# Optimization experiments

Measured on AMD Instinct MI355X. Metric: run time of the kernel, lower is better.

## Reference

```python
import jax, jax.numpy as jnp
import numpy as np

THETA = 10000.0

def _rope(x, cos, sin):
    # x: [B, S, D]; cos/sin: [S, D/2]. Pairs are (x[..., 2i], x[..., 2i+1]) treated as complex.
    xr = x.reshape(*x.shape[:-1], -1, 2)
    x0, x1 = xr[..., 0], xr[..., 1]
    o0 = x0 * cos - x1 * sin
    o1 = x0 * sin + x1 * cos
    return jnp.stack([o0, o1], axis=-1).reshape(x.shape)

def setup_inputs() -> dict:
    key = jax.random.key(0)
    ks = jax.random.split(key, 7)
    B, S, D = 4, 2048, 1024
    sd = 1.0 / np.sqrt(D)
    return {
        "x": jax.random.normal(ks[0], (B, S, D), dtype=jnp.float32),
        "wq_w": jax.random.normal(ks[1], (D, D), dtype=jnp.float32) * sd,
        "wq_b": jax.random.normal(ks[2], (D,), dtype=jnp.float32) * 0.01,
        "wk_w": jax.random.normal(ks[3], (D, D), dtype=jnp.float32) * sd,
        "wk_b": jax.random.normal(ks[4], (D,), dtype=jnp.float32) * 0.01,
        "wv_w": jax.random.normal(ks[5], (D, D), dtype=jnp.float32) * sd,
        "wv_b": jax.random.normal(ks[6], (D,), dtype=jnp.float32) * 0.01,
    }

def reference(x, wq_w, wq_b, wk_w, wk_b, wv_w, wv_b):
    B, S, D = x.shape
    # QKV projections (torch Linear: y = x @ W.T + b)
    q = jnp.einsum('bsd,ed->bse', x, wq_w) + wq_b
    k = jnp.einsum('bsd,ed->bse', x, wk_w) + wk_b
    v = jnp.einsum('bsd,ed->bse', x, wv_w) + wv_b
    # Rotary embedding: freqs_cis[t, i] = exp(i * t / theta^(2i/D))
    inv_freq = 1.0 / (THETA ** (jnp.arange(0, D, 2, dtype=jnp.float32) / D))  # [D/2]
    ang = jnp.arange(S, dtype=jnp.float32)[:, None] * inv_freq[None, :]  # [S, D/2]
    cos, sin = jnp.cos(ang), jnp.sin(ang)
    q = _rope(q, cos, sin)
    k = _rope(k, cos, sin)
    # Full (non-causal, single-head) attention with scale 1/sqrt(dim)
    scores = jnp.einsum('bqd,bkd->bqk', q, k) / jnp.sqrt(jnp.float32(D))
    probs = jax.nn.softmax(scores.astype(jnp.float32), axis=-1)
    return jnp.einsum('bqk,bkd->bqd', probs, v)
```

## Files before the change

### kernel.cpp

```cpp
#include <hip/hip_runtime.h>
#include <cstdint>

using u16 = unsigned short;
using u32 = unsigned int;

typedef __attribute__((ext_vector_type(8))) short short8;
typedef __attribute__((ext_vector_type(4))) float floatx4;

__device__ __forceinline__ u16 f2bf(float f) {
    u32 u = __float_as_uint(f);
    u32 r = u + 0x7fffu + ((u >> 16) & 1u);
    return (u16)(r >> 16);
}

__global__ void cvt_all(const float* __restrict__ x, u16* __restrict__ xb,
                        const float* __restrict__ w0, const float* __restrict__ w1,
                        const float* __restrict__ w2,
                        u16* __restrict__ o0, u16* __restrict__ o1, u16* __restrict__ o2,
                        const float* __restrict__ qb, const float* __restrict__ kb,
                        float* __restrict__ bqk, float* __restrict__ rowsum)
{
    int b = blockIdx.x;
    if (b >= 11272) {
        long i = ((long)(b - 11272) * 256 + threadIdx.x) * 4;
        *reinterpret_cast<float4*>(rowsum + i) = make_float4(0.f, 0.f, 0.f, 0.f);
        return;
    }
    if (b >= 11264) {
        int i = (b - 11264) * 256 + threadIdx.x;
        bqk[i] = (i < 1024) ? qb[i] : kb[i - 1024];
        return;
    }
    const float* src; u16* dst; long base;
    if (b < 8192) { src = x; dst = xb; base = (long)b; }
    else {
        int r = b - 8192, seg = r >> 10;
        if (seg == 0)      { src = w0; dst = o0; }
        else if (seg == 1) { src = w1; dst = o1; }
        else               { src = w2; dst = o2; }
        base = (long)(r & 1023);
    }
    long i = (base * 256 + threadIdx.x) * 4;
    float4 v = *reinterpret_cast<const float4*>(src + i);
    uint2 o;
    o.x = (u32)f2bf(v.x) | ((u32)f2bf(v.y) << 16);
    o.y = (u32)f2bf(v.z) | ((u32)f2bf(v.w) << 16);
    *reinterpret_cast<uint2*>(dst + i) = o;
}

__device__ __forceinline__ void async_cp16(const u16* g, u16* l) {
    __builtin_amdgcn_global_load_lds(
        (const __attribute__((address_space(1))) void*)g,
        (__attribute__((address_space(3))) void*)l, 16, 0, 0);
}

#define MEMFENCE asm volatile("" ::: "memory")
__device__ __forceinline__ void barrier_raw() {
    MEMFENCE; __builtin_amdgcn_s_barrier(); MEMFENCE;
}
__device__ __forceinline__ void vmwait(int n) {
    if      (n == 6) asm volatile("s_waitcnt vmcnt(6)" ::: "memory");
    else if (n == 4) asm volatile("s_waitcnt vmcnt(4)" ::: "memory");
    else if (n == 2) asm volatile("s_waitcnt vmcnt(2)" ::: "memory");
    else if (n == 0) asm volatile("s_waitcnt vmcnt(0)" ::: "memory");
}

template <bool BF16_OUT, bool EXPOUT>
__device__ __forceinline__ void gemm_core(
    const u16* __restrict__ A, const u16* __restrict__ B, void* __restrict__ Cv,
    int K, int lda, int ldb, int ldc,
    long tile_m, long tile_n, long cbase,
    const float* bias_col, const float* bias_row,
    float scale, bool rope, float* __restrict__ rowsum,
    const float* __restrict__ rowscale, u16* smem)
{
    u16* As = smem;
    u16* Bs = smem + 8192;

    const int tid  = threadIdx.x;
    const int lane = tid & 63;
    const int wave = tid >> 6;
    const int wm = (wave >> 1) << 6;
    const int wn = (wave & 1) << 6;

    floatx4 acc[4][4] = {};

    const int srow = tid >> 2;
    const int skp  = (((tid & 3) ^ (srow & 3))) * 8;
    const u16* Ag = A + (tile_m + srow) * (long)lda + skp;
    const u16* Bg = B + (tile_n + srow) * (long)ldb + skp;
    u16* Asl = &As[tid * 8];
    u16* Bsl = &Bs[tid * 8];

    const int fm  = lane & 15;
    const int fks = (((lane >> 4) ^ (lane & 3))) * 8;

    for (int k0 = 0; k0 < K; k0 += 64) {
        async_cp16(Ag,                       Asl);
        async_cp16(Ag + 64 * (long)lda,      Asl + 64 * 32);
        async_cp16(Ag + 32,                  Asl + 4096);
        async_cp16(Ag + 32 + 64 * (long)lda, Asl + 4096 + 64 * 32);
        async_cp16(Bg,                       Bsl);
        async_cp16(Bg + 64 * (long)ldb,      Bsl + 64 * 32);
        async_cp16(Bg + 32,                  Bsl + 4096);
        async_cp16(Bg + 32 + 64 * (long)ldb, Bsl + 4096 + 64 * 32);
        Ag += 64; Bg += 64;
        __syncthreads();

        #pragma unroll
        for (int c = 0; c < 2; ++c) {
            const u16* Ap = As + c * 4096;
            const u16* Bp = Bs + c * 4096;
            short8 af[4], bfr[4];
            #pragma unroll
            for (int i = 0; i < 4; ++i)
                af[i] = *reinterpret_cast<const short8*>(&Ap[(wm + i * 16 + fm) * 32 + fks]);
            #pragma unroll
            for (int j = 0; j < 4; ++j)
                bfr[j] = *reinterpret_cast<const short8*>(&Bp[(wn + j * 16 + fm) * 32 + fks]);
            #pragma unroll
            for (int i = 0; i < 4; ++i)
                #pragma unroll
                for (int j = 0; j < 4; ++j)
                    acc[i][j] = __builtin_amdgcn_mfma_f32_16x16x32_bf16(af[i], bfr[j], acc[i][j], 0, 0, 0);
        }
        __syncthreads();
    }

    const int q4  = lane >> 4;
    const int c16 = lane & 15;
    float* smemf  = (float*)smem;
    float* myeps = smemf + wave * (16 * 68);
    const long n0 = tile_n + wn + c16 * 4;

    float4 bc4 = make_float4(0.f, 0.f, 0.f, 0.f);
    if (bias_col) bc4 = *reinterpret_cast<const float4*>(bias_col + n0);

    float inv0 = 0.f, inv1 = 0.f;
    if (rope) {
        int p0 = (int)(n0 >> 1);
        inv0 = __expf((float)(p0 & 511)       * -1.79889463e-2f);
        inv1 = __expf((float)((p0 + 1) & 511) * -1.79889463e-2f);
    }

    #pragma unroll
    for (int i = 0; i < 4; ++i) {
        #pragma unroll
        for (int j = 0; j < 4; ++j)
            #pragma unroll
            for (int r = 0; r < 4; ++r)
                myeps[(q4 * 4 + r) * 68 + j * 16 + c16] = acc[i][j][r];
        __syncthreads();
        #pragma unroll
        for (int p = 0; p < 4; ++p) {
            int lrow = p * 4 + q4;
            long m = tile_m + wm + i * 16 + lrow;
            float4 v = *reinterpret_cast<const float4*>(&myeps[lrow * 68 + c16 * 4]);
            float sc = scale;
            if (rowscale) sc *= 1.0f / rowscale[m];
            v.x = v.x * sc + bc4.x;
            v.y = v.y * sc + bc4.y;
            v.z = v.z * sc + bc4.z;
            v.w = v.w * sc + bc4.w;
            if (bias_row) {
                float br = bias_row[m];
                v.x += br; v.y += br; v.z += br; v.w += br;
            }
            if (rope) {
                int s = (int)(m & 2047);
                float a0 = (float)s * inv0, a1 = (float)s * inv1;
                float sn0 = __sinf(a0), cs0 = __cosf(a0);
                float sn1 = __sinf(a1), cs1 = __cosf(a1);
                float x0 = v.x, x1 = v.y, x2 = v.z, x3 = v.w;
                v.x = x0 * cs0 - x1 * sn0;
                v.y = x0 * sn0 + x1 * cs0;
                v.z = x2 * cs1 - x3 * sn1;
                v.w = x2 * sn1 + x3 * cs1;
            }
            if constexpr (EXPOUT) {
                v.x = __expf(v.x); v.y = __expf(v.y);
                v.z = __expf(v.z); v.w = __expf(v.w);
                float s4 = v.x + v.y + v.z + v.w;
                s4 += __shfl_xor(s4, 1);
                s4 += __shfl_xor(s4, 2);
                s4 += __shfl_xor(s4, 4);
                s4 += __shfl_xor(s4, 8);
                if (c16 == 0) atomicAdd(&rowsum[m], s4);
            }
            long off = cbase + m * (long)ldc + n0;
            if constexpr (BF16_OUT) {
                uint2 o;
                o.x = (u32)f2bf(v.x) | ((u32)f2bf(v.y) << 16);
                o.y = (u32)f2bf(v.z) | ((u32)f2bf(v.w) << 16);
                *reinterpret_cast<uint2*>((u16*)Cv + off) = o;
            } else {
                *reinterpret_cast<float4*>((float*)Cv + off) = v;
            }
        }
        __syncthreads();
    }
}

template <bool BF16_OUT, bool EXPOUT>
__device__ __forceinline__ void gemm8_core(
    const u16* __restrict__ A, const u16* __restrict__ B, void* __restrict__ Cv,
    int K, int lda, int ldb, int ldc,
    long tile_m, long tile_n, long cbase,
    const float* __restrict__ bias_col, const float* __restrict__ bias_row,
    float scale, bool rope, float* __restrict__ rowsum, u16* smem)
{
    const int tid  = threadIdx.x;
    const int lane = tid & 63;
    const int wave = tid >> 6;
    const int wm2  = (wave >> 2) * 128;
    const int wn2  = (wave & 3) * 64;
    const int fm   = lane & 15;
    const int fks  = (((lane >> 4) ^ ((lane >> 1) & 3))) * 8;

    const int srow = tid >> 2;
    const int kgl  = ((tid & 3) ^ ((tid >> 3) & 3)) * 8;
    const u16* Asrc = A + (tile_m + srow) * (long)lda + kgl;
    const u16* Bsrc = B + (tile_n + srow) * (long)ldb + kgl;
    u16* dst0 = smem + tid * 8;

    const int U = K >> 5;

    floatx4 acc[8][4] = {};
    short8 bf[4];

    auto stageA = [&](int v) {
        u16* d = dst0 + ((2 * v) & 7) * 8192;
        const u16* s = Asrc + v * 32;
        async_cp16(s, d);
        async_cp16(s + 128 * (long)lda, d + 4096);
    };
    auto stageB = [&](int v) {
        u16* d = dst0 + ((2 * v + 1) & 7) * 8192;
        const u16* s = Bsrc + v * 32;
        async_cp16(s, d);
        async_cp16(s + 128 * (long)ldb, d + 4096);
    };

    auto phase_pair = [&](int u, int vmx, bool stb, bool sta)
        __attribute__((always_inline))
    {
        const u16* Ap = smem + ((2 * u) & 7) * 8192;
        const u16* Bp = smem + ((2 * u + 1) & 7) * 8192;
        short8 af[4];
        #pragma unroll
        for (int i = 0; i < 4; ++i)
            af[i] = *reinterpret_cast<const short8*>(&Ap[(wm2 + i * 16 + fm) * 32 + fks]);
        #pragma unroll
        for (int j = 0; j < 4; ++j)
            bf[j] = *reinterpret_cast<const short8*>(&Bp[(wn2 + j * 16 + fm) * 32 + fks]);
        if (stb) stageB(u + 2);
        vmwait(vmx);
        barrier_raw();
        __builtin_amdgcn_sched_barrier(0);
        __builtin_amdgcn_s_setprio(1);
        #pragma unroll
        for (int i = 0; i < 4; ++i)
            #pragma unroll
            for (int j = 0; j < 4; ++j)
                acc[i][j] = __builtin_amdgcn_mfma_f32_16x16x32_bf16(af[i], bf[j], acc[i][j], 0, 0, 0);
        __builtin_amdgcn_s_setprio(0);
        __builtin_amdgcn_sched_barrier(0);
        barrier_raw();
        #pragma unroll
        for (int i = 0; i < 4; ++i)
            af[i] = *reinterpret_cast<const short8*>(&Ap[(wm2 + 64 + i * 16 + fm) * 32 + fks]);
        if (sta) stageA(u + 3);
        barrier_raw();
        __builtin_amdgcn_sched_barrier(0);
        __builtin_amdgcn_s_setprio(1);
        #pragma unroll
        for (int i = 0; i < 4; ++i)
            #pragma unroll
            for (int j = 0; j < 4; ++j)
                acc[4 + i][j] = __builtin_amdgcn_mfma_f32_16x16x32_bf16(af[i], bf[j], acc[4 + i][j], 0, 0, 0);
        __builtin_amdgcn_s_setprio(0);
        __builtin_amdgcn_sched_barrier(0);
        barrier_raw();
    };

    stageA(0); stageB(0); stageA(1); stageB(1); stageA(2);
    vmwait(6);
    barrier_raw();

    for (int u = 0; u + 3 < U; ++u)
        phase_pair(u, 6, true, true);
    phase_pair(U - 3, 6, true,  false);
    phase_pair(U - 2, 2, false, false);
    phase_pair(U - 1, 0, false, false);

    const int q4  = lane >> 4;
    const int c16 = lane & 15;
    float* smemf  = (float*)smem;
    float* myeps  = smemf + wave * (16 * 68);
    const long n0 = tile_n + wn2 + c16 * 4;

    float4 bc4 = make_float4(0.f, 0.f, 0.f, 0.f);
    if (bias_col) bc4 = *reinterpret_cast<const float4*>(bias_col + n0);

    float inv0 = 0.f, inv1 = 0.f;
    if (rope) {
        int p0 = (int)(n0 >> 1);
        inv0 = __expf((float)(p0 & 511)       * -1.79889463e-2f);
        inv1 = __expf((float)((p0 + 1) & 511) * -1.79889463e-2f);
    }

    #pragma unroll
    for (int i = 0; i < 8; ++i) {
        #pragma unroll
        for (int j = 0; j < 4; ++j)
            #pragma unroll
            for (int r = 0; r < 4; ++r)
                myeps[(q4 * 4 + r) * 68 + j * 16 + c16] = acc[i][j][r];
        __syncthreads();
        #pragma unroll
        for (int p = 0; p < 4; ++p) {
            int lrow = p * 4 + q4;
            long m = tile_m + wm2 + i * 16 + lrow;
            float4 v = *reinterpret_cast<const float4*>(&myeps[lrow * 68 + c16 * 4]);
            v.x = v.x * scale + bc4.x;
            v.y = v.y * scale + bc4.y;
            v.z = v.z * scale + bc4.z;
            v.w = v.w * scale + bc4.w;
            if (bias_row) {
                float br = bias_row[m];
                v.x += br; v.y += br; v.z += br; v.w += br;
            }
            if (rope) {
                int s = (int)(m & 2047);
                float a0 = (float)s * inv0, a1 = (float)s * inv1;
                float sn0 = __sinf(a0), cs0 = __cosf(a0);
                float sn1 = __sinf(a1), cs1 = __cosf(a1);
                float x0 = v.x, x1 = v.y, x2 = v.z, x3 = v.w;
                v.x = x0 * cs0 - x1 * sn0;
                v.y = x0 * sn0 + x1 * cs0;
                v.z = x2 * cs1 - x3 * sn1;
                v.w = x2 * sn1 + x3 * cs1;
            }
            if constexpr (EXPOUT) {
                v.x = __expf(v.x); v.y = __expf(v.y);
                v.z = __expf(v.z); v.w = __expf(v.w);
                float s4 = v.x + v.y + v.z + v.w;
                s4 += __shfl_xor(s4, 1);
                s4 += __shfl_xor(s4, 2);
                s4 += __shfl_xor(s4, 4);
                s4 += __shfl_xor(s4, 8);
                if (c16 == 0) atomicAdd(&rowsum[m], s4);
            }
            long off = cbase + m * (long)ldc + n0;
            if constexpr (BF16_OUT) {
                uint2 o;
                o.x = (u32)f2bf(v.x) | ((u32)f2bf(v.y) << 16);
                o.y = (u32)f2bf(v.z) | ((u32)f2bf(v.w) << 16);
                *reinterpret_cast<uint2*>((u16*)Cv + off) = o;
            } else {
                *reinterpret_cast<float4*>((float*)Cv + off) = v;
            }
        }
        __syncthreads();
    }
}

__global__ __launch_bounds__(256, 4)
void gemm_fused12(const u16* __restrict__ xb, const u16* __restrict__ wqk,
                  const u16* __restrict__ wv, u16* __restrict__ QK, u16* __restrict__ VT,
                  const float* __restrict__ bqk, const float* __restrict__ wvb)
{
    u32 id = blockIdx.x;
    id = (id & 7u) * 192u + (id >> 3);
    __shared__ alignas(16) u16 smem[16384];
    if (id < 1024u) {
        u32 bx = id & 15u, by = id >> 4;
        gemm_core<true, false>(xb, wqk, QK, 1024, 1024, 1024, 2048,
                        (long)by * 128, (long)bx * 128, 0L,
                        bqk, nullptr, 1.0f, true, nullptr, nullptr, smem);
    } else {
        u32 r = id - 1024u;
        u32 bx = r & 15u, by = (r >> 4) & 7u, bz = r >> 7;
        gemm_core<true, false>(wv, xb + (long)bz * 2048 * 1024, VT,
                        1024, 1024, 1024, 2048,
                        (long)by * 128, (long)bx * 128, (long)bz * 1024 * 2048,
                        nullptr, wvb, 1.0f, false, nullptr, nullptr, smem);
    }
}

__global__ __launch_bounds__(512, 2)
void gemm8_qkt(const u16* __restrict__ QK, u16* __restrict__ Pbuf,
               float* __restrict__ rsum)
{
    u32 id = blockIdx.x;
    id = (id & 7u) * 32u + (id >> 3);
    u32 bz = id >> 6, q = id & 63u, bx = q & 7u, by = q >> 3;
    __shared__ alignas(16) u16 smem[65536];
    const u16* base = QK + (long)bz * 2048 * 2048;
    gemm8_core<true, true>(base, base + 1024, Pbuf, 1024, 2048, 2048, 2048,
                           nullptr == nullptr ? (long)by * 256 : 0, (long)bx * 256,
                           (long)bz * 2048 * 2048,
                           nullptr, nullptr, 0.03125f, false,
                           rsum + (long)bz * 2048, smem);
}

__global__ __launch_bounds__(256, 4)
void gemm_pv(const u16* __restrict__ Pbuf, const u16* __restrict__ VT,
             float* __restrict__ out, const float* __restrict__ rsum)
{
    u32 ord = blockIdx.x;
    u32 x  = ord & 7u;
    u32 n  = ord >> 3;
    u32 bz = x >> 1;
    u32 by = (x & 1u) * 8u + (n >> 3);
    u32 bx = n & 7u;
    __shared__ alignas(16) u16 smem[16384];
    gemm_core<false, false>(Pbuf + (long)bz * 2048 * 2048,
                            VT   + (long)bz * 1024 * 2048,
                            out, 2048, 2048, 2048, 1024,
                            (long)by * 128, (long)bx * 128, (long)bz * 2048 * 1024,
                            nullptr, nullptr, 1.0f, false, nullptr,
                            rsum + (long)bz * 2048, smem);
}

extern "C" void kernel_launch(void* const* d_in, const int* in_sizes, int n_in,
                              void* d_out, int out_size, void* d_ws, size_t ws_size,
                              hipStream_t stream)
{
    const float* x   = (const float*)d_in[0];
    const float* wqw = (const float*)d_in[1];
    const float* wqb = (const float*)d_in[2];
    const float* wkw = (const float*)d_in[3];
    const float* wkb = (const float*)d_in[4];
    const float* wvw = (const float*)d_in[5];
    const float* wvb = (const float*)d_in[6];
    float* out = (float*)d_out;

    char* ws = (char*)d_ws;
    const size_t MB = 1ull << 20;
    u16*   Pbuf = (u16*)(ws + 64 * MB);
    u16*   QK   = (u16*)(ws + 96 * MB);
    u16*   VT   = (u16*)(ws + 128 * MB);
    float* rsum = (float*)(ws + 144 * MB);
    u16*   xb    = (u16*)(ws + 0);
    u16*   wqk   = (u16*)(ws + 16 * MB);
    u16*   wvbuf = (u16*)(ws + 20 * MB);
    float* bqk   = (float*)(ws + 22 * MB);

    cvt_all<<<dim3(11280), 256, 0, stream>>>(x, xb, wqw, wkw, wvw,
                                             wqk, wqk + 1024 * 1024, wvbuf,
                                             wqb, wkb, bqk, rsum);

    gemm_fused12<<<dim3(1536), 256, 0, stream>>>(xb, wqk, wvbuf, QK, VT, bqk, wvb);

    gemm8_qkt<<<dim3(256), 512, 0, stream>>>(QK, Pbuf, rsum);

    gemm_pv<<<dim3(512), 256, 0, stream>>>(Pbuf, VT, out, rsum);

    (void)in_sizes; (void)n_in; (void)out_size; (void)ws_size;
}
```

Before: 259.1 us.

## Replace PV GEMM with 8-wave 256x128 tile kernel using 4-stage async pipeline

Replaces the 128x128, 256-thread PV GEMM with a new 512-thread core that computes 256x128 tiles. It uses a four-buffer global_load_lds pipeline, split A/B staging and two MFMA half-phases per k-step, plus wave priority boosts. The larger tile is meant to cut global and LDS traffic per FLOP and hide load latency better. The cost is fewer blocks (256 instead of 512), which lowers occupancy and may cause tail imbalance across CUs.

```diff
diff --git a/kernel.cpp b/kernel.cpp
--- a/kernel.cpp
+++ b/kernel.cpp
@@ -60,7 +60,9 @@
 }
 __device__ __forceinline__ void vmwait(int n) {
     if      (n == 6) asm volatile("s_waitcnt vmcnt(6)" ::: "memory");
+    else if (n == 5) asm volatile("s_waitcnt vmcnt(5)" ::: "memory");
     else if (n == 4) asm volatile("s_waitcnt vmcnt(4)" ::: "memory");
+    else if (n == 3) asm volatile("s_waitcnt vmcnt(3)" ::: "memory");
     else if (n == 2) asm volatile("s_waitcnt vmcnt(2)" ::: "memory");
     else if (n == 0) asm volatile("s_waitcnt vmcnt(0)" ::: "memory");
 }
@@ -360,6 +362,120 @@
             } else {
                 *reinterpret_cast<float4*>((float*)Cv + off) = v;
             }
+        }
+        __syncthreads();
+    }
+}
+
+__device__ __forceinline__ void gemm8n128_core(
+    const u16* __restrict__ A, const u16* __restrict__ B, float* __restrict__ C,
+    int K, int lda, int ldb, int ldc,
+    long tile_m, long tile_n, long cbase,
+    const float* __restrict__ rowscale, u16* smem)
+{
+    const int tid  = threadIdx.x;
+    const int lane = tid & 63;
+    const int wave = tid >> 6;
+    const int wm2  = (wave >> 2) * 128;
+    const int wn2  = (wave & 3) * 32;
+    const int fm   = lane & 15;
+    const int fks  = (((lane >> 4) ^ ((lane >> 1) & 3))) * 8;
+
+    const int srow = tid >> 2;
+    const int kgl  = ((tid & 3) ^ ((tid >> 3) & 3)) * 8;
+    const u16* Asrc = A + (tile_m + srow) * (long)lda + kgl;
+    const u16* Bsrc = B + (tile_n + srow) * (long)ldb + kgl;
+    u16* dst0 = smem + tid * 8;
+
+    const int U = K >> 5;
+
+    floatx4 acc[8][2] = {};
+    short8 bf[2];
+
+    auto stageA = [&](int v) {
+        u16* d = dst0 + (v & 3) * 12288;
+        const u16* s = Asrc + v * 32;
+        async_cp16(s, d);
+        async_cp16(s + 128 * (long)lda, d + 4096);
+    };
+    auto stageB = [&](int v) {
+        async_cp16(Bsrc + v * 32, dst0 + (v & 3) * 12288 + 8192);
+    };
+
+    auto phase_pair = [&](int u, int vmx, bool stb, bool sta)
+        __attribute__((always_inline))
+    {
+        const u16* Ap = smem + (u & 3) * 12288;
+        const u16* Bp = Ap + 8192;
+        short8 af[4];
+        #pragma unroll
+        for (int i = 0; i < 4; ++i)
+            af[i] = *reinterpret_cast<const short8*>(&Ap[(wm2 + i * 16 + fm) * 32 + fks]);
+        #pragma unroll
+        for (int j = 0; j < 2; ++j)
+            bf[j] = *reinterpret_cast<const short8*>(&Bp[(wn2 + j * 16 + fm) * 32 + fks]);
+        if (stb) stageB(u + 2);
+        vmwait(vmx);
+        barrier_raw();
+        __builtin_amdgcn_sched_barrier(0);
+        __builtin_amdgcn_s_setprio(1);
+        #pragma unroll
+        for (int i = 0; i < 4; ++i)
+            #pragma unroll
+            for (int j = 0; j < 2; ++j)
+                acc[i][j] = __builtin_amdgcn_mfma_f32_16x16x32_bf16(af[i], bf[j], acc[i][j], 0, 0, 0);
+        __builtin_amdgcn_s_setprio(0);
+        __builtin_amdgcn_sched_barrier(0);
+        barrier_raw();
+        #pragma unroll
+        for (int i = 0; i < 4; ++i)
+            af[i] = *reinterpret_cast<const short8*>(&Ap[(wm2 + 64 + i * 16 + fm) * 32 + fks]);
+        if (sta) stageA(u + 3);
+        barrier_raw();
+        __builtin_amdgcn_sched_barrier(0);
+        __builtin_amdgcn_s_setprio(1);
+        #pragma unroll
+        for (int i = 0; i < 4; ++i)
+            #pragma unroll
+            for (int j = 0; j < 2; ++j)
+                acc[4 + i][j] = __builtin_amdgcn_mfma_f32_16x16x32_bf16(af[i], bf[j], acc[4 + i][j], 0, 0, 0);
+        __builtin_amdgcn_s_setprio(0);
+        __builtin_amdgcn_sched_barrier(0);
+        barrier_raw();
+    };
+
+    stageA(0); stageB(0); stageA(1); stageB(1); stageA(2);
+    vmwait(5);
+    barrier_raw();
+
+    for (int u = 0; u + 3 < U; ++u)
+        phase_pair(u, 3, true, true);
+    phase_pair(U - 3, 3, true,  false);
+    phase_pair(U - 2, 0, false, false);
+    phase_pair(U - 1, 0, false, false);
+
+    const int q4  = lane >> 4;
+    const int c16 = lane & 15;
+    float* smemf = (float*)smem;
+    float* myeps = smemf + wave * (16 * 36);
+    const long n0 = tile_n + wn2 + c16 * 2;
+
+    #pragma unroll
+    for (int i = 0; i < 8; ++i) {
+        #pragma unroll
+        for (int j = 0; j < 2; ++j)
+            #pragma unroll
+            for (int r = 0; r < 4; ++r)
+                myeps[(q4 * 4 + r) * 36 + j * 16 + c16] = acc[i][j][r];
+        __syncthreads();
+        #pragma unroll
+        for (int p = 0; p < 4; ++p) {
+            int lrow = p * 4 + q4;
+            long m = tile_m + wm2 + i * 16 + lrow;
+            float2 v = *reinterpret_cast<const float2*>(&myeps[lrow * 36 + c16 * 2]);
+            float sc = 1.0f / rowscale[m];
+            v.x *= sc; v.y *= sc;
+            *reinterpret_cast<float2*>(C + cbase + m * (long)ldc + n0) = v;
         }
         __syncthreads();
     }
@@ -398,29 +514,24 @@
     __shared__ alignas(16) u16 smem[65536];
     const u16* base = QK + (long)bz * 2048 * 2048;
     gemm8_core<true, true>(base, base + 1024, Pbuf, 1024, 2048, 2048, 2048,
-                           nullptr == nullptr ? (long)by * 256 : 0, (long)bx * 256,
-                           (long)bz * 2048 * 2048,
+                           (long)by * 256, (long)bx * 256, (long)bz * 2048 * 2048,
                            nullptr, nullptr, 0.03125f, false,
                            rsum + (long)bz * 2048, smem);
 }
 
-__global__ __launch_bounds__(256, 4)
-void gemm_pv(const u16* __restrict__ Pbuf, const u16* __restrict__ VT,
-             float* __restrict__ out, const float* __restrict__ rsum)
-{
-    u32 ord = blockIdx.x;
-    u32 x  = ord & 7u;
-    u32 n  = ord >> 3;
-    u32 bz = x >> 1;
-    u32 by = (x & 1u) * 8u + (n >> 3);
-    u32 bx = n & 7u;
-    __shared__ alignas(16) u16 smem[16384];
-    gemm_core<false, false>(Pbuf + (long)bz * 2048 * 2048,
-                            VT   + (long)bz * 1024 * 2048,
-                            out, 2048, 2048, 2048, 1024,
-                            (long)by * 128, (long)bx * 128, (long)bz * 2048 * 1024,
-                            nullptr, nullptr, 1.0f, false, nullptr,
-                            rsum + (long)bz * 2048, smem);
+__global__ __launch_bounds__(512, 2)
+void gemm8_pv(const u16* __restrict__ Pbuf, const u16* __restrict__ VT,
+              float* __restrict__ out, const float* __restrict__ rsum)
+{
+    u32 id = blockIdx.x;
+    id = (id & 7u) * 32u + (id >> 3);
+    u32 bz = id >> 6, q = id & 63u, by = q >> 3, bx = q & 7u;
+    __shared__ alignas(16) u16 smem[49152];
+    gemm8n128_core(Pbuf + (long)bz * 2048 * 2048,
+                   VT   + (long)bz * 1024 * 2048,
+                   out, 2048, 2048, 2048, 1024,
+                   (long)by * 256, (long)bx * 128, (long)bz * 2048 * 1024,
+                   rsum + (long)bz * 2048, smem);
 }
 
 extern "C" void kernel_launch(void* const* d_in, const int* in_sizes, int n_in,
@@ -455,7 +566,7 @@
 
     gemm8_qkt<<<dim3(256), 512, 0, stream>>>(QK, Pbuf, rsum);
 
-    gemm_pv<<<dim3(512), 256, 0, stream>>>(Pbuf, VT, out, rsum);
+    gemm8_pv<<<dim3(256), 512, 0, stream>>>(Pbuf, VT, out, rsum);
 
     (void)in_sizes; (void)n_in; (void)out_size; (void)ws_size;
 }
```

New measurement: 236.7 us. 8.6% less time.
